# Kernel tuning notes

Measured on AMD Instinct MI355X. Metric: run time of the kernel, lower is better.

Reference implementation:

```python
import jax, jax.numpy as jnp
import numpy as np

N_NODES = 100000
DEG = 16   # regular-graph degree -> every per-node subgraph is a (DEG+1)-node star
DIM = 128


def _crelu(z):
    return (jax.nn.relu(z.real) + 1j * jax.nn.relu(z.imag)).astype(jnp.complex64)


def _evolution_row(deg, tr, ti):
    # get_node_adjacency keeps only edges incident to the center node, so A_i is the
    # star graph K_{1,deg} with the center at index 0 -- identical for every node of a
    # deg-regular graph, so U is computed once.
    n = deg + 1
    A = jnp.zeros((n, n), jnp.complex64).at[0, 1:].set(1.0).at[1:, 0].set(1.0)
    t = (tr + 1j * ti).astype(jnp.complex64)
    G = jax.scipy.linalg.expm(-1j * A * t)
    # torch: sqrt(max eigval of G G^dagger); G G^dagger is Hermitian PSD -> eigvalsh
    s = jnp.sqrt(jnp.max(jnp.linalg.eigvalsh(G @ G.conj().T))).astype(jnp.complex64)
    Lt = G / s
    # np.sqrt on a matrix is ELEMENTWISE sqrt in the torch code -- replicate that
    Rt = jnp.sqrt(jnp.eye(n, dtype=jnp.complex64) - Lt @ (G.conj().T / s))
    # torch converts complex_time via .item() into numpy: no grad through U
    return jax.lax.stop_gradient(Lt[0] + Rt[0])  # (deg+1,) complex row 0 of [[Lt,Rt],[Rt,-Lt]]


def _layer(h, nbrs, Wr, Wi, br, bi, tr, ti, ebr, ebi):
    W = (Wr + 1j * Wi).astype(jnp.complex64)
    b = (br + 1j * bi).astype(jnp.complex64)
    h = _crelu(h @ W.T + b)
    deg = nbrs.shape[1]
    w = _evolution_row(deg, tr, ti)
    # evolved[0] = w[0]*h_i + sum_k w[1+k]*h_{sorted_nbr_k(i)}
    out = w[0] * h
    for k in range(deg):  # fixed small unrolled loop; avoids a [N, deg+1, C] intermediate
        out = out + w[1 + k] * h[nbrs[:, k]]
    return out + (ebr + 1j * ebi).astype(jnp.complex64)


def setup_inputs():
    key = jax.random.key(0)
    ks = jax.random.split(key, 12)
    x = jax.random.normal(ks[0], (N_NODES, DIM), jnp.float32)
    # circulant DEG-regular graph: node i ~ i +/- k (mod N), k=1..DEG/2; each undirected edge once
    K = DEG // 2
    i = np.arange(N_NODES)
    src = np.repeat(i, K)
    dst = ((i[:, None] + np.arange(1, K + 1)[None, :]) % N_NODES).reshape(-1)
    edge_index = jnp.asarray(np.stack([src, dst]), dtype=jnp.int32)
    sc = 0.05
    d = {"x": x, "edge_index": edge_index}
    for l, k0 in ((1, 1), (2, 6)):
        d[f"W{l}r"] = jax.random.normal(ks[k0], (DIM, DIM), jnp.float32) * sc
        d[f"W{l}i"] = jax.random.normal(ks[k0 + 1], (DIM, DIM), jnp.float32) * sc
        d[f"b{l}r"] = jax.random.normal(ks[k0 + 2], (DIM,), jnp.float32) * sc
        d[f"b{l}i"] = jax.random.normal(ks[k0 + 3], (DIM,), jnp.float32) * sc
        d[f"t{l}r"] = jnp.float32(1.0)
        d[f"t{l}i"] = jnp.float32(0.0)
        d[f"eb{l}r"] = jnp.zeros((DIM,), jnp.float32)
        d[f"eb{l}i"] = jnp.zeros((DIM,), jnp.float32)
    return d


def reference(x, edge_index, W1r, W1i, b1r, b1i, t1r, t1i, eb1r, eb1i,
              W2r, W2i, b2r, b2i, t2r, t2i, eb2r, eb2i):
    N = x.shape[0]
    src, dst = edge_index[0], edge_index[1]
    nodes = jnp.concatenate([src, dst])
    nbr = jnp.concatenate([dst, src])
    order = jnp.lexsort((nbr, nodes))        # sorted neighbor list per node
    deg = nodes.shape[0] // N                # regular graph -> static degree
    nbrs = nbr[order].reshape(N, deg)        # [N, DEG]
    h = x.astype(jnp.complex64)              # prepare_complex_input
    h = _layer(h, nbrs, W1r, W1i, b1r, b1i, t1r, t1i, eb1r, eb1i)
    h = _layer(h, nbrs, W2r, W2i, b2r, b2i, t2r, t2i, eb2r, eb2i)
    return h.real                            # output_type='real'
```

## Files before the change

kernel.cpp:

```cpp
#include <hip/hip_runtime.h>
#include <hip/hip_bf16.h>
#include <stdint.h>

typedef __attribute__((ext_vector_type(8))) short bf8_t;
typedef __attribute__((ext_vector_type(4))) float f32x4_t;
typedef __attribute__((ext_vector_type(4))) unsigned short us4_t;

#define MFMA_BF16 __builtin_amdgcn_mfma_f32_16x16x32_bf16

__device__ __forceinline__ unsigned short f2bf(float f) {
  union { float f; unsigned u; } x; x.f = f;
  unsigned r = (x.u + 0x7FFFu + ((x.u >> 16) & 1u)) >> 16;
  return (unsigned short)r;
}
__device__ __forceinline__ float bf2f(unsigned short b) {
  union { unsigned u; float f; } x; x.u = ((unsigned)b) << 16;
  return x.f;
}

__global__ void compute_wscal(const float* t1r, const float* t1i,
                              const float* t2r, const float* t2i,
                              float* wsc, int deg) {
  if (threadIdx.x != 0 || blockIdx.x != 0) return;
  float r = sqrtf((float)deg);
  for (int l = 0; l < 2; ++l) {
    float tr = l ? t2r[0] : t1r[0];
    float ti = l ? t2i[0] : t1i[0];
    float x = r * tr, y = r * ti;
    float cr = cosf(x) * coshf(y), ci = -sinf(x) * sinhf(y);
    float sr = sinf(x) * coshf(y), si = cosf(x) * sinhf(y);
    float a = cr * cr + ci * ci + sr * sr + si * si;
    float b = -2.0f * (ci * sr - cr * si);
    float s2 = fmaxf(a + fabsf(b), 1.0f);
    float s = sqrtf(s2);
    float l0r = cr / s, l0i = ci / s;
    float l1r = si / (r * s), l1i = -sr / (r * s);
    float q0 = 1.0f - a / s2;
    float r0r = (q0 >= 0.0f) ? sqrtf(q0) : 0.0f;
    float r0i = (q0 >= 0.0f) ? 0.0f : sqrtf(-q0);
    float q1 = -b / (r * s2);
    float r1r = (q1 >= 0.0f) ? sqrtf(q1) : 0.0f;
    float r1i = (q1 >= 0.0f) ? 0.0f : sqrtf(-q1);
    wsc[l * 4 + 0] = l0r + r0r;
    wsc[l * 4 + 1] = l0i + r0i;
    wsc[l * 4 + 2] = l1r + r1r;
    wsc[l * 4 + 3] = l1i + r1i;
  }
}

__device__ __forceinline__ void store_side(int* __restrict__ cnt,
                                           int* __restrict__ nbrs,
                                           int deg, int key, int val) {
  unsigned long long remaining = __ballot(1);
  unsigned long long mymask = 0;
  while (remaining) {
    int lead = __ffsll((long long)remaining) - 1;
    int lkey = __shfl(key, lead);
    unsigned long long m = __ballot(key == lkey);
    if (key == lkey) mymask = m;
    remaining &= ~m;
  }
  const int lane = threadIdx.x & 63;
  const int leader = __ffsll((long long)mymask) - 1;
  int base = 0;
  if (lane == leader) base = atomicAdd(&cnt[key], __popcll(mymask));
  base = __shfl(base, leader);
  const int rank = __popcll(mymask & ((1ull << lane) - 1ull));
  nbrs[(long)key * deg + base + rank] = val;
}

__global__ __launch_bounds__(256) void build_nbrs(
    const int* __restrict__ ei, int E, int* __restrict__ cnt,
    int* __restrict__ nbrs, int deg) {
  int e = blockIdx.x * 256 + threadIdx.x;
  if (e >= E) return;
  int s = ei[e], d = ei[E + e];
  store_side(cnt, nbrs, deg, s, d);
  store_side(cnt, nbrs, deg, d, s);
}

__device__ __forceinline__ void stage_w(unsigned char* ldsW,
                                        const float* __restrict__ Wr,
                                        const float* __restrict__ Wi, int tid) {
#pragma unroll
  for (int p = 0; p < 2; ++p) {
    const float* src = p ? Wi : Wr;
#pragma unroll
    for (int i = 0; i < 4; ++i) {
      const int e8 = (i * 512 + tid) * 8;
      float4 a = *(const float4*)(src + e8);
      float4 b = *(const float4*)(src + e8 + 4);
      union { bf8_t v; unsigned short s[8]; } o;
      o.s[0] = f2bf(a.x); o.s[1] = f2bf(a.y); o.s[2] = f2bf(a.z); o.s[3] = f2bf(a.w);
      o.s[4] = f2bf(b.x); o.s[5] = f2bf(b.y); o.s[6] = f2bf(b.z); o.s[7] = f2bf(b.w);
      const int c = e8 >> 7, k = e8 & 127;
      const int byte = p * 32768 + c * 256 + ((k * 2) ^ ((c & 7) << 4));
      *(bf8_t*)(ldsW + byte) = o.v;
    }
  }
}

__global__ __launch_bounds__(512) void gemm_l1(
    const float* __restrict__ Xf,
    const float* __restrict__ Wr, const float* __restrict__ Wi,
    const float* __restrict__ br, const float* __restrict__ bi,
    unsigned short* __restrict__ Or, unsigned short* __restrict__ Oi, int n) {
  __shared__ unsigned char ldsW[65536];
  const int tid = threadIdx.x;
  stage_w(ldsW, Wr, Wi, tid);
  __syncthreads();

  const int wv = tid >> 6, lane = tid & 63;
  const int fr = lane & 15, kg = lane >> 4;
  const int rowbase = blockIdx.x * 128 + wv * 16;
  const int node = min(rowbase + fr, n - 1);
  const long a_off = (long)node * 128;

  bf8_t a[4];
#pragma unroll
  for (int ks = 0; ks < 4; ++ks) {
    const int koff = ks * 32 + kg * 8;
    float4 u = *(const float4*)(Xf + a_off + koff);
    float4 v = *(const float4*)(Xf + a_off + koff + 4);
    union { bf8_t vv; unsigned short s[8]; } t;
    t.s[0] = f2bf(u.x); t.s[1] = f2bf(u.y); t.s[2] = f2bf(u.z); t.s[3] = f2bf(u.w);
    t.s[4] = f2bf(v.x); t.s[5] = f2bf(v.y); t.s[6] = f2bf(v.z); t.s[7] = f2bf(v.w);
    a[ks] = t.vv;
  }

  const int onode = rowbase + fr;
  const long obase = (long)onode * 128;
#pragma unroll
  for (int cf = 0; cf < 8; ++cf) {
    const int c = cf * 16 + fr;
    const int cbyte = c * 256, swz = (c & 7) << 4;
    f32x4_t accr = (f32x4_t)0.0f, acci = (f32x4_t)0.0f;
#pragma unroll
    for (int ks = 0; ks < 4; ++ks) {
      const int kb = (ks * 32 + kg * 8) * 2;
      bf8_t w_r = *(const bf8_t*)(ldsW + cbyte + (kb ^ swz));
      bf8_t w_i = *(const bf8_t*)(ldsW + 32768 + cbyte + (kb ^ swz));
      accr = MFMA_BF16(w_r, a[ks], accr, 0, 0, 0);
      acci = MFMA_BF16(w_i, a[ks], acci, 0, 0, 0);
    }
    if (onode < n) {
      const int cb = cf * 16 + kg * 4;
      union { float4 f4; float f[4]; } b4r, b4i;
      b4r.f4 = *(const float4*)(br + cb);
      b4i.f4 = *(const float4*)(bi + cb);
      us4_t pr, pi;
#pragma unroll
      for (int j = 0; j < 4; ++j) {
        pr[j] = f2bf(fmaxf(accr[j] + b4r.f[j], 0.0f));
        pi[j] = f2bf(fmaxf(acci[j] + b4i.f[j], 0.0f));
      }
      *(us4_t*)(Or + obase + cb) = pr;
      *(us4_t*)(Oi + obase + cb) = pi;
    }
  }
}

template <int DEG>
__global__ __launch_bounds__(512) void fused_l2(
    const unsigned short* __restrict__ h1r, const unsigned short* __restrict__ h1i,
    const int* __restrict__ nbrs, const float* __restrict__ wsc,
    const float* __restrict__ eb1r, const float* __restrict__ eb1i,
    const float* __restrict__ W2r, const float* __restrict__ W2i,
    const float* __restrict__ b2r, const float* __restrict__ b2i,
    unsigned short* __restrict__ Or, unsigned short* __restrict__ Oi,
    int n, int deg_rt) {
  __shared__ unsigned char ldsW[65536];
  const int tid = threadIdx.x;
  stage_w(ldsW, W2r, W2i, tid);
  __syncthreads();

  const int wv = tid >> 6, lane = tid & 63;
  const int fr = lane & 15, kg = lane >> 4;
  const int rowbase = blockIdx.x * 128 + wv * 16;
  const int node = min(rowbase + fr, n - 1);
  const long a_off = (long)node * 128;
  const float w0r = wsc[0], w0i = wsc[1], w1r = wsc[2], w1i = wsc[3];
  const int deg = DEG ? DEG : deg_rt;
  const int* nbp = nbrs + (long)node * deg;

  int nb[DEG ? DEG : 1];
  if (DEG) {
#pragma unroll
    for (int j = 0; j < (DEG ? DEG : 1); ++j) nb[j] = nbp[j];
  }

  bf8_t ar[4], ai[4], ain[4];
#pragma unroll
  for (int ks = 0; ks < 4; ++ks) {
    const int koff = ks * 32 + kg * 8;
    union { bf8_t v; unsigned short s[8]; } o_r, o_i;
    o_r.v = *(const bf8_t*)(h1r + a_off + koff);
    o_i.v = *(const bf8_t*)(h1i + a_off + koff);
    float sr[8], si[8];
#pragma unroll
    for (int e = 0; e < 8; ++e) { sr[e] = 0.0f; si[e] = 0.0f; }
    if (DEG) {
#pragma unroll
      for (int j = 0; j < (DEG ? DEG : 1); ++j) {
        const long m = (long)nb[j] * 128 + koff;
        union { bf8_t v; unsigned short s[8]; } vr2, vi2;
        vr2.v = *(const bf8_t*)(h1r + m);
        vi2.v = *(const bf8_t*)(h1i + m);
#pragma unroll
        for (int e = 0; e < 8; ++e) { sr[e] += bf2f(vr2.s[e]); si[e] += bf2f(vi2.s[e]); }
      }
    } else {
      for (int j = 0; j < deg; ++j) {
        const long m = (long)nbp[j] * 128 + koff;
        union { bf8_t v; unsigned short s[8]; } vr2, vi2;
        vr2.v = *(const bf8_t*)(h1r + m);
        vi2.v = *(const bf8_t*)(h1i + m);
#pragma unroll
        for (int e = 0; e < 8; ++e) { sr[e] += bf2f(vr2.s[e]); si[e] += bf2f(vi2.s[e]); }
      }
    }
    union { float4 f4; float f[4]; } er0, er1, ei0, ei1;
    er0.f4 = *(const float4*)(eb1r + koff);
    er1.f4 = *(const float4*)(eb1r + koff + 4);
    ei0.f4 = *(const float4*)(eb1i + koff);
    ei1.f4 = *(const float4*)(eb1i + koff + 4);
    union { bf8_t v; unsigned short s[8]; } pr, pi;
#pragma unroll
    for (int e = 0; e < 8; ++e) {
      float hr = bf2f(o_r.s[e]), hi = bf2f(o_i.s[e]);
      float ebR = (e < 4) ? er0.f[e] : er1.f[e - 4];
      float ebI = (e < 4) ? ei0.f[e] : ei1.f[e - 4];
      float gr = w0r * hr - w0i * hi + w1r * sr[e] - w1i * si[e] + ebR;
      float gi = w0r * hi + w0i * hr + w1r * si[e] + w1i * sr[e] + ebI;
      pr.s[e] = f2bf(gr); pi.s[e] = f2bf(gi);
    }
    ar[ks] = pr.v; ai[ks] = pi.v;
    union { bf8_t v; unsigned u[4]; } t; t.v = pi.v;
#pragma unroll
    for (int q = 0; q < 4; ++q) t.u[q] ^= 0x80008000u;
    ain[ks] = t.v;
  }

  const int onode = rowbase + fr;
  const long obase = (long)onode * 128;
#pragma unroll
  for (int cf = 0; cf < 8; ++cf) {
    const int c = cf * 16 + fr;
    const int cbyte = c * 256, swz = (c & 7) << 4;
    f32x4_t accr = (f32x4_t)0.0f, acci = (f32x4_t)0.0f;
#pragma unroll
    for (int ks = 0; ks < 4; ++ks) {
      const int kb = (ks * 32 + kg * 8) * 2;
      bf8_t w_r = *(const bf8_t*)(ldsW + cbyte + (kb ^ swz));
      bf8_t w_i = *(const bf8_t*)(ldsW + 32768 + cbyte + (kb ^ swz));
      accr = MFMA_BF16(w_r, ar[ks], accr, 0, 0, 0);
      accr = MFMA_BF16(w_i, ain[ks], accr, 0, 0, 0);
      acci = MFMA_BF16(w_i, ar[ks], acci, 0, 0, 0);
      acci = MFMA_BF16(w_r, ai[ks], acci, 0, 0, 0);
    }
    if (onode < n) {
      const int cb = cf * 16 + kg * 4;
      union { float4 f4; float f[4]; } b4r, b4i;
      b4r.f4 = *(const float4*)(b2r + cb);
      b4i.f4 = *(const float4*)(b2i + cb);
      us4_t pr, pi;
#pragma unroll
      for (int j = 0; j < 4; ++j) {
        pr[j] = f2bf(fmaxf(accr[j] + b4r.f[j], 0.0f));
        pi[j] = f2bf(fmaxf(acci[j] + b4i.f[j], 0.0f));
      }
      *(us4_t*)(Or + obase + cb) = pr;
      *(us4_t*)(Oi + obase + cb) = pi;
    }
  }
}

template <int DEG>
__global__ __launch_bounds__(256) void agg_final(
    const unsigned short* __restrict__ hr, const unsigned short* __restrict__ hi,
    const int* __restrict__ nbrs, const float* __restrict__ wsc,
    const float* __restrict__ ebr,
    float* __restrict__ outf, int n, int deg_rt) {
  const int g = blockIdx.x * 256 + threadIdx.x;
  const int node = g >> 4;
  if (node >= n) return;
  const int ch0 = (g & 15) * 8;
  const int deg = DEG ? DEG : deg_rt;
  const float w0r = wsc[0], w0i = wsc[1], w1r = wsc[2], w1i = wsc[3];

  union { bf8_t v; unsigned short s[8]; } ur, ui;
  ur.v = *(const bf8_t*)(hr + (long)node * 128 + ch0);
  ui.v = *(const bf8_t*)(hi + (long)node * 128 + ch0);
  float srf[8], sif[8];
#pragma unroll
  for (int e = 0; e < 8; ++e) { srf[e] = 0.0f; sif[e] = 0.0f; }
  const int* nbp = nbrs + (long)node * deg;
  if (DEG) {
#pragma unroll
    for (int k = 0; k < (DEG ? DEG : 1); ++k) {
      const long m = (long)nbp[k] * 128 + ch0;
      union { bf8_t v; unsigned short s[8]; } vr2, vi2;
      vr2.v = *(const bf8_t*)(hr + m);
      vi2.v = *(const bf8_t*)(hi + m);
#pragma unroll
      for (int e = 0; e < 8; ++e) { srf[e] += bf2f(vr2.s[e]); sif[e] += bf2f(vi2.s[e]); }
    }
  } else {
    for (int k = 0; k < deg; ++k) {
      const long m = (long)nbp[k] * 128 + ch0;
      union { bf8_t v; unsigned short s[8]; } vr2, vi2;
      vr2.v = *(const bf8_t*)(hr + m);
      vi2.v = *(const bf8_t*)(hi + m);
#pragma unroll
      for (int e = 0; e < 8; ++e) { srf[e] += bf2f(vr2.s[e]); sif[e] += bf2f(vi2.s[e]); }
    }
  }
  union { float4 f4; float f[4]; } o0, o1;
#pragma unroll
  for (int e = 0; e < 8; ++e) {
    const int c = ch0 + e;
    float hrf = bf2f(ur.s[e]), hif = bf2f(ui.s[e]);
    float R = w0r * hrf - w0i * hif + w1r * srf[e] - w1i * sif[e] + ebr[c];
    if (e < 4) o0.f[e] = R; else o1.f[e - 4] = R;
  }
  *(float4*)(outf + (long)node * 128 + ch0) = o0.f4;
  *(float4*)(outf + (long)node * 128 + ch0 + 4) = o1.f4;
}

extern "C" void kernel_launch(void* const* d_in, const int* in_sizes, int n_in,
                              void* d_out, int out_size, void* d_ws, size_t ws_size,
                              hipStream_t stream) {
  const float* x    = (const float*)d_in[0];
  const int*   ei   = (const int*)d_in[1];
  const float* W1r  = (const float*)d_in[2];
  const float* W1i  = (const float*)d_in[3];
  const float* b1r  = (const float*)d_in[4];
  const float* b1i  = (const float*)d_in[5];
  const float* t1r  = (const float*)d_in[6];
  const float* t1i  = (const float*)d_in[7];
  const float* eb1r = (const float*)d_in[8];
  const float* eb1i = (const float*)d_in[9];
  const float* W2r  = (const float*)d_in[10];
  const float* W2i  = (const float*)d_in[11];
  const float* b2r  = (const float*)d_in[12];
  const float* b2i  = (const float*)d_in[13];
  const float* t2r  = (const float*)d_in[14];
  const float* t2i  = (const float*)d_in[15];
  const float* eb2r = (const float*)d_in[16];
  const float* eb2i = (const float*)d_in[17];

  const int DIM = 128;
  const int N = in_sizes[0] / DIM;
  const int E = in_sizes[1] / 2;
  const int deg = (2 * E) / N;

  char* ws = (char*)d_ws;
  size_t off = 0;
  auto alloc = [&](size_t bytes) -> char* {
    char* p = ws + off;
    off += (bytes + 255) & ~(size_t)255;
    return p;
  };
  int* cnt  = (int*)alloc((size_t)N * 4);
  int* nbrs = (int*)alloc((size_t)N * deg * 4);
  float* wsc = (float*)alloc(8 * 4);
  const size_t nH = (size_t)N * DIM;
  unsigned short* h1r = (unsigned short*)alloc(nH * 2);
  unsigned short* h1i = (unsigned short*)alloc(nH * 2);
  unsigned short* h2r = (unsigned short*)alloc(nH * 2);
  unsigned short* h2i = (unsigned short*)alloc(nH * 2);
  (void)ws_size; (void)n_in; (void)out_size;

  hipMemsetAsync(cnt, 0, (size_t)N * 4, stream);
  build_nbrs<<<(E + 255) / 256, 256, 0, stream>>>(ei, E, cnt, nbrs, deg);
  compute_wscal<<<1, 64, 0, stream>>>(t1r, t1i, t2r, t2i, wsc, deg);

  const int gemm_blocks = (N + 127) / 128;
  const int agg_blocks = (N * 16 + 255) / 256;

  gemm_l1<<<gemm_blocks, 512, 0, stream>>>(x, W1r, W1i, b1r, b1i, h1r, h1i, N);

  if (deg == 16) {
    fused_l2<16><<<gemm_blocks, 512, 0, stream>>>(h1r, h1i, nbrs, wsc, eb1r, eb1i,
                                                  W2r, W2i, b2r, b2i, h2r, h2i, N, deg);
    agg_final<16><<<agg_blocks, 256, 0, stream>>>(h2r, h2i, nbrs, wsc + 4, eb2r,
                                                  (float*)d_out, N, deg);
  } else {
    fused_l2<0><<<gemm_blocks, 512, 0, stream>>>(h1r, h1i, nbrs, wsc, eb1r, eb1i,
                                                 W2r, W2i, b2r, b2i, h2r, h2i, N, deg);
    agg_final<0><<<agg_blocks, 256, 0, stream>>>(h2r, h2i, nbrs, wsc + 4, eb2r,
                                                 (float*)d_out, N, deg);
  }
}
```

Before: 400.3 us.

## Interleave real/imag bf16 chunks in one buffer and swizzle blocks across XCDs

New measurement: 338.8 us. 1.18x faster.

```diff
diff --git a/kernel.cpp b/kernel.cpp
--- a/kernel.cpp
+++ b/kernel.cpp
@@ -16,6 +16,14 @@
 __device__ __forceinline__ float bf2f(unsigned short b) {
   union { unsigned u; float f; } x; x.u = ((unsigned)b) << 16;
   return x.f;
+}
+
+__device__ __forceinline__ int xcd_swizzle(int b, int nwg) {
+  const int NX = 8;
+  int q = nwg / NX, r = nwg % NX;
+  int xcd = b % NX, idx = b / NX;
+  int start = (xcd < r) ? xcd * (q + 1) : r * (q + 1) + (xcd - r) * q;
+  return start + idx;
 }
 
 __global__ void compute_wscal(const float* t1r, const float* t1i,
@@ -100,11 +108,12 @@
   }
 }
 
+
 __global__ __launch_bounds__(512) void gemm_l1(
     const float* __restrict__ Xf,
     const float* __restrict__ Wr, const float* __restrict__ Wi,
     const float* __restrict__ br, const float* __restrict__ bi,
-    unsigned short* __restrict__ Or, unsigned short* __restrict__ Oi, int n) {
+    unsigned short* __restrict__ H1, int n) {
   __shared__ unsigned char ldsW[65536];
   const int tid = threadIdx.x;
   stage_w(ldsW, Wr, Wi, tid);
@@ -112,7 +121,8 @@
 
   const int wv = tid >> 6, lane = tid & 63;
   const int fr = lane & 15, kg = lane >> 4;
-  const int rowbase = blockIdx.x * 128 + wv * 16;
+  const int lb = xcd_swizzle(blockIdx.x, gridDim.x);
+  const int rowbase = lb * 128 + wv * 16;
   const int node = min(rowbase + fr, n - 1);
   const long a_off = (long)node * 128;
 
@@ -129,7 +139,7 @@
   }
 
   const int onode = rowbase + fr;
-  const long obase = (long)onode * 128;
+  const long obase = (long)onode * 256;
 #pragma unroll
   for (int cf = 0; cf < 8; ++cf) {
     const int c = cf * 16 + fr;
@@ -145,6 +155,7 @@
     }
     if (onode < n) {
       const int cb = cf * 16 + kg * 4;
+      const int chunk = cb >> 3, sub = cb & 7;
       union { float4 f4; float f[4]; } b4r, b4i;
       b4r.f4 = *(const float4*)(br + cb);
       b4i.f4 = *(const float4*)(bi + cb);
@@ -154,21 +165,20 @@
         pr[j] = f2bf(fmaxf(accr[j] + b4r.f[j], 0.0f));
         pi[j] = f2bf(fmaxf(acci[j] + b4i.f[j], 0.0f));
       }
-      *(us4_t*)(Or + obase + cb) = pr;
-      *(us4_t*)(Oi + obase + cb) = pi;
+      *(us4_t*)(H1 + obase + chunk * 16 + sub) = pr;
+      *(us4_t*)(H1 + obase + chunk * 16 + 8 + sub) = pi;
     }
   }
 }
 
 template <int DEG>
 __global__ __launch_bounds__(512) void fused_l2(
-    const unsigned short* __restrict__ h1r, const unsigned short* __restrict__ h1i,
+    const unsigned short* __restrict__ H1,
     const int* __restrict__ nbrs, const float* __restrict__ wsc,
     const float* __restrict__ eb1r, const float* __restrict__ eb1i,
     const float* __restrict__ W2r, const float* __restrict__ W2i,
     const float* __restrict__ b2r, const float* __restrict__ b2i,
-    unsigned short* __restrict__ Or, unsigned short* __restrict__ Oi,
-    int n, int deg_rt) {
+    unsigned short* __restrict__ H2, int n, int deg_rt) {
   __shared__ unsigned char ldsW[65536];
   const int tid = threadIdx.x;
   stage_w(ldsW, W2r, W2i, tid);
@@ -176,9 +186,9 @@
 
   const int wv = tid >> 6, lane = tid & 63;
   const int fr = lane & 15, kg = lane >> 4;
-  const int rowbase = blockIdx.x * 128 + wv * 16;
+  const int lb = xcd_swizzle(blockIdx.x, gridDim.x);
+  const int rowbase = lb * 128 + wv * 16;
   const int node = min(rowbase + fr, n - 1);
-  const long a_off = (long)node * 128;
   const float w0r = wsc[0], w0i = wsc[1], w1r = wsc[2], w1i = wsc[3];
   const int deg = DEG ? DEG : deg_rt;
   const int* nbp = nbrs + (long)node * deg;
@@ -192,33 +202,34 @@
   bf8_t ar[4], ai[4], ain[4];
 #pragma unroll
   for (int ks = 0; ks < 4; ++ks) {
-    const int koff = ks * 32 + kg * 8;
+    const int ch16 = (ks * 4 + kg) * 16;
     union { bf8_t v; unsigned short s[8]; } o_r, o_i;
-    o_r.v = *(const bf8_t*)(h1r + a_off + koff);
-    o_i.v = *(const bf8_t*)(h1i + a_off + koff);
+    o_r.v = *(const bf8_t*)(H1 + (long)node * 256 + ch16);
+    o_i.v = *(const bf8_t*)(H1 + (long)node * 256 + ch16 + 8);
     float sr[8], si[8];
 #pragma unroll
     for (int e = 0; e < 8; ++e) { sr[e] = 0.0f; si[e] = 0.0f; }
     if (DEG) {
 #pragma unroll
       for (int j = 0; j < (DEG ? DEG : 1); ++j) {
-        const long m = (long)nb[j] * 128 + koff;
+        const long m = (long)nb[j] * 256 + ch16;
         union { bf8_t v; unsigned short s[8]; } vr2, vi2;
-        vr2.v = *(const bf8_t*)(h1r + m);
-        vi2.v = *(const bf8_t*)(h1i + m);
+        vr2.v = *(const bf8_t*)(H1 + m);
+        vi2.v = *(const bf8_t*)(H1 + m + 8);
 #pragma unroll
         for (int e = 0; e < 8; ++e) { sr[e] += bf2f(vr2.s[e]); si[e] += bf2f(vi2.s[e]); }
       }
     } else {
       for (int j = 0; j < deg; ++j) {
-        const long m = (long)nbp[j] * 128 + koff;
+        const long m = (long)nbp[j] * 256 + ch16;
         union { bf8_t v; unsigned short s[8]; } vr2, vi2;
-        vr2.v = *(const bf8_t*)(h1r + m);
-        vi2.v = *(const bf8_t*)(h1i + m);
+        vr2.v = *(const bf8_t*)(H1 + m);
+        vi2.v = *(const bf8_t*)(H1 + m + 8);
 #pragma unroll
         for (int e = 0; e < 8; ++e) { sr[e] += bf2f(vr2.s[e]); si[e] += bf2f(vi2.s[e]); }
       }
     }
+    const int koff = ks * 32 + kg * 8;
     union { float4 f4; float f[4]; } er0, er1, ei0, ei1;
     er0.f4 = *(const float4*)(eb1r + koff);
     er1.f4 = *(const float4*)(eb1r + koff + 4);
@@ -242,7 +253,7 @@
   }
 
   const int onode = rowbase + fr;
-  const long obase = (long)onode * 128;
+  const long obase = (long)onode * 256;
 #pragma unroll
   for (int cf = 0; cf < 8; ++cf) {
     const int c = cf * 16 + fr;
@@ -260,6 +271,7 @@
     }
     if (onode < n) {
       const int cb = cf * 16 + kg * 4;
+      const int chunk = cb >> 3, sub = cb & 7;
       union { float4 f4; float f[4]; } b4r, b4i;
       b4r.f4 = *(const float4*)(b2r + cb);
       b4i.f4 = *(const float4*)(b2i + cb);
@@ -269,28 +281,30 @@
         pr[j] = f2bf(fmaxf(accr[j] + b4r.f[j], 0.0f));
         pi[j] = f2bf(fmaxf(acci[j] + b4i.f[j], 0.0f));
       }
-      *(us4_t*)(Or + obase + cb) = pr;
-      *(us4_t*)(Oi + obase + cb) = pi;
+      *(us4_t*)(H2 + obase + chunk * 16 + sub) = pr;
+      *(us4_t*)(H2 + obase + chunk * 16 + 8 + sub) = pi;
     }
   }
 }
 
 template <int DEG>
 __global__ __launch_bounds__(256) void agg_final(
-    const unsigned short* __restrict__ hr, const unsigned short* __restrict__ hi,
+    const unsigned short* __restrict__ H2,
     const int* __restrict__ nbrs, const float* __restrict__ wsc,
     const float* __restrict__ ebr,
     float* __restrict__ outf, int n, int deg_rt) {
-  const int g = blockIdx.x * 256 + threadIdx.x;
+  const int lb = xcd_swizzle(blockIdx.x, gridDim.x);
+  const int g = lb * 256 + threadIdx.x;
   const int node = g >> 4;
   if (node >= n) return;
-  const int ch0 = (g & 15) * 8;
+  const int g2 = g & 15;
+  const int ch0 = g2 * 8;
   const int deg = DEG ? DEG : deg_rt;
   const float w0r = wsc[0], w0i = wsc[1], w1r = wsc[2], w1i = wsc[3];
 
   union { bf8_t v; unsigned short s[8]; } ur, ui;
-  ur.v = *(const bf8_t*)(hr + (long)node * 128 + ch0);
-  ui.v = *(const bf8_t*)(hi + (long)node * 128 + ch0);
+  ur.v = *(const bf8_t*)(H2 + (long)node * 256 + g2 * 16);
+  ui.v = *(const bf8_t*)(H2 + (long)node * 256 + g2 * 16 + 8);
   float srf[8], sif[8];
 #pragma unroll
   for (int e = 0; e < 8; ++e) { srf[e] = 0.0f; sif[e] = 0.0f; }
@@ -298,19 +312,19 @@
   if (DEG) {
 #pragma unroll
     for (int k = 0; k < (DEG ? DEG : 1); ++k) {
-      const long m = (long)nbp[k] * 128 + ch0;
+      const long m = (long)nbp[k] * 256 + g2 * 16;
       union { bf8_t v; unsigned short s[8]; } vr2, vi2;
-      vr2.v = *(const bf8_t*)(hr + m);
-      vi2.v = *(const bf8_t*)(hi + m);
+      vr2.v = *(const bf8_t*)(H2 + m);
+      vi2.v = *(const bf8_t*)(H2 + m + 8);
 #pragma unroll
       for (int e = 0; e < 8; ++e) { srf[e] += bf2f(vr2.s[e]); sif[e] += bf2f(vi2.s[e]); }
     }
   } else {
     for (int k = 0; k < deg; ++k) {
-      const long m = (long)nbp[k] * 128 + ch0;
+      const long m = (long)nbp[k] * 256 + g2 * 16;
       union { bf8_t v; unsigned short s[8]; } vr2, vi2;
-      vr2.v = *(const bf8_t*)(hr + m);
-      vi2.v = *(const bf8_t*)(hi + m);
+      vr2.v = *(const bf8_t*)(H2 + m);
+      vi2.v = *(const bf8_t*)(H2 + m + 8);
 #pragma unroll
       for (int e = 0; e < 8; ++e) { srf[e] += bf2f(vr2.s[e]); sif[e] += bf2f(vi2.s[e]); }
     }
@@ -365,10 +379,8 @@
   int* nbrs = (int*)alloc((size_t)N * deg * 4);
   float* wsc = (float*)alloc(8 * 4);
   const size_t nH = (size_t)N * DIM;
-  unsigned short* h1r = (unsigned short*)alloc(nH * 2);
-  unsigned short* h1i = (unsigned short*)alloc(nH * 2);
-  unsigned short* h2r = (unsigned short*)alloc(nH * 2);
-  unsigned short* h2i = (unsigned short*)alloc(nH * 2);
+  unsigned short* h1 = (unsigned short*)alloc(nH * 4);
+  unsigned short* h2 = (unsigned short*)alloc(nH * 4);
   (void)ws_size; (void)n_in; (void)out_size;
 
   hipMemsetAsync(cnt, 0, (size_t)N * 4, stream);
@@ -378,17 +390,17 @@
   const int gemm_blocks = (N + 127) / 128;
   const int agg_blocks = (N * 16 + 255) / 256;
 
-  gemm_l1<<<gemm_blocks, 512, 0, stream>>>(x, W1r, W1i, b1r, b1i, h1r, h1i, N);
+  gemm_l1<<<gemm_blocks, 512, 0, stream>>>(x, W1r, W1i, b1r, b1i, h1, N);
 
   if (deg == 16) {
-    fused_l2<16><<<gemm_blocks, 512, 0, stream>>>(h1r, h1i, nbrs, wsc, eb1r, eb1i,
-                                                  W2r, W2i, b2r, b2i, h2r, h2i, N, deg);
-    agg_final<16><<<agg_blocks, 256, 0, stream>>>(h2r, h2i, nbrs, wsc + 4, eb2r,
+    fused_l2<16><<<gemm_blocks, 512, 0, stream>>>(h1, nbrs, wsc, eb1r, eb1i,
+                                                  W2r, W2i, b2r, b2i, h2, N, deg);
+    agg_final<16><<<agg_blocks, 256, 0, stream>>>(h2, nbrs, wsc + 4, eb2r,
                                                   (float*)d_out, N, deg);
   } else {
-    fused_l2<0><<<gemm_blocks, 512, 0, stream>>>(h1r, h1i, nbrs, wsc, eb1r, eb1i,
-                                                 W2r, W2i, b2r, b2i, h2r, h2i, N, deg);
-    agg_final<0><<<agg_blocks, 256, 0, stream>>>(h2r, h2i, nbrs, wsc + 4, eb2r,
+    fused_l2<0><<<gemm_blocks, 512, 0, stream>>>(h1, nbrs, wsc, eb1r, eb1i,
+                                                 W2r, W2i, b2r, b2i, h2, N, deg);
+    agg_final<0><<<agg_blocks, 256, 0, stream>>>(h2, nbrs, wsc + 4, eb2r,
                                                  (float*)d_out, N, deg);
   }
 }
```
